# Kernel optimization log

Measured on AMD Instinct MI355X. Metric: run time of the kernel, lower is better.

The kernel has to match this reference:

```python
import jax, jax.numpy as jnp
import numpy as np

N_CODES = 8192
CODE_DIM = 256


def setup_inputs() -> dict:
    key = jax.random.key(0)
    kx, ke = jax.random.split(key)
    x = jax.random.normal(kx, (16, 4096, CODE_DIM), dtype=jnp.float32)
    # nn.Embedding weight initialized uniform(-1/n, 1/n)
    emb = jax.random.uniform(ke, (N_CODES, CODE_DIM), dtype=jnp.float32,
                             minval=-1.0 / N_CODES, maxval=1.0 / N_CODES)
    return {"x": x, "emb": emb}


def reference(x, emb):
    B, T, D = x.shape
    flat = x.reshape(-1, D)                                   # [BT, D]
    # squared euclidean distance: ||f||^2 - 2 f.e^T + ||e||^2  -> [BT, N]
    dist = ((flat * flat).sum(axis=1, keepdims=True)
            - 2.0 * flat @ emb.T
            + (emb * emb).sum(axis=1))
    idx = jnp.argmin(dist, axis=1)                            # [BT] int
    quant = emb[idx].reshape(x.shape)                         # [B, T, D]
    # commitment-style loss: mse(stop_grad(quant), x)
    loss = jnp.mean(jnp.square(jax.lax.stop_gradient(quant) - x))
    # straight-through estimator
    y = x + jax.lax.stop_gradient(quant - x)
    return y, idx.reshape(B, T), loss
```

## Files before the change

kernel.cpp:

```cpp
#include <hip/hip_runtime.h>
#include <stdint.h>


#define NCODES 8192
#define DDIM   256
#define BT     65536

#define TM     128
#define TN     128
#define NSEG   256
#define F4S    17

#define CAPC   48
#define MARGIN 7e-4f
#define TOKPB  128
#define CCODES 64
#define CHUNKS 128
#define KSCALE 1048576.0f
#define KOFF   131072.0f
#define KMARG  737

typedef float  f32x4  __attribute__((ext_vector_type(4)));
typedef __bf16 bf16x8 __attribute__((ext_vector_type(8)));

#define GLDS16(g, l) __builtin_amdgcn_global_load_lds(                         \
    (const __attribute__((address_space(1))) void*)(g),                        \
    (__attribute__((address_space(3))) void*)(l), 16, 0, 0)
#define GLDS4(g, l) __builtin_amdgcn_global_load_lds(                          \
    (const __attribute__((address_space(1))) void*)(g),                        \
    (__attribute__((address_space(3))) void*)(l), 4, 0, 0)

__device__ __forceinline__ unsigned int fenc(float f) {
  unsigned int u = __float_as_uint(f);
  return (u & 0x80000000u) ? ~u : (u | 0x80000000u);
}
__device__ __forceinline__ float fdec(unsigned int u) {
  unsigned int v = (u & 0x80000000u) ? (u ^ 0x80000000u) : ~u;
  return __uint_as_float(v);
}

__device__ __forceinline__ float np_pairwise256_sq(const float4* __restrict__ row) {
#pragma clang fp contract(off)
  float half[2];
  #pragma unroll
  for (int h = 0; h < 2; h++) {
    float r0,r1,r2,r3,r4,r5,r6,r7;
    float4 q0 = row[h*32 + 0];
    float4 q1 = row[h*32 + 1];
    r0 = q0.x*q0.x; r1 = q0.y*q0.y; r2 = q0.z*q0.z; r3 = q0.w*q0.w;
    r4 = q1.x*q1.x; r5 = q1.y*q1.y; r6 = q1.z*q1.z; r7 = q1.w*q1.w;
    #pragma unroll
    for (int g = 1; g < 16; g++) {
      q0 = row[h*32 + g*2];
      q1 = row[h*32 + g*2 + 1];
      r0 += q0.x*q0.x; r1 += q0.y*q0.y; r2 += q0.z*q0.z; r3 += q0.w*q0.w;
      r4 += q1.x*q1.x; r5 += q1.y*q1.y; r6 += q1.z*q1.z; r7 += q1.w*q1.w;
    }
    half[h] = ((r0+r1) + (r2+r3)) + ((r4+r5) + (r6+r7));
  }
  return half[0] + half[1];
}

__device__ __forceinline__ float np_pairwise256_sq_s(const float* __restrict__ row) {
#pragma clang fp contract(off)
  float half[2];
  #pragma unroll
  for (int h = 0; h < 2; h++) {
    const float* p = row + h * 128;
    float r0,r1,r2,r3,r4,r5,r6,r7;
    r0 = p[0]*p[0]; r1 = p[1]*p[1]; r2 = p[2]*p[2]; r3 = p[3]*p[3];
    r4 = p[4]*p[4]; r5 = p[5]*p[5]; r6 = p[6]*p[6]; r7 = p[7]*p[7];
    #pragma unroll
    for (int g = 1; g < 16; g++) {
      const float* q = p + g * 8;
      r0 += q[0]*q[0]; r1 += q[1]*q[1]; r2 += q[2]*q[2]; r3 += q[3]*q[3];
      r4 += q[4]*q[4]; r5 += q[5]*q[5]; r6 += q[6]*q[6]; r7 += q[7]*q[7];
    }
    half[h] = ((r0+r1) + (r2+r3)) + ((r4+r5) + (r6+r7));
  }
  return half[0] + half[1];
}

__device__ __forceinline__ float exact_score(const float* __restrict__ xr,
                                             const float4* __restrict__ er,
                                             float Ar, float Cv) {
#pragma clang fp contract(off)
  float b = 0.0f;
  #pragma unroll 8
  for (int q = 0; q < 64; ++q) {
    float4 ev = er[q];
    b = fmaf(xr[q * 4 + 0], ev.x, b);
    b = fmaf(xr[q * 4 + 1], ev.y, b);
    b = fmaf(xr[q * 4 + 2], ev.z, b);
    b = fmaf(xr[q * 4 + 3], ev.w, b);
  }
  const float t1 = fmaf(-2.0f, b, Ar);
  return t1 + Cv;
}

__device__ __forceinline__ void exact_score2(const float* __restrict__ xr,
                                             const float4* __restrict__ e1,
                                             const float4* __restrict__ e2,
                                             float Ar, float Cv1, float Cv2,
                                             float& s1, float& s2) {
#pragma clang fp contract(off)
  float b1 = 0.0f, b2 = 0.0f;
  #pragma unroll 8
  for (int q = 0; q < 64; ++q) {
    const float4 v1 = e1[q], v2 = e2[q];
    const float x0 = xr[q * 4 + 0], x1 = xr[q * 4 + 1];
    const float x2 = xr[q * 4 + 2], x3 = xr[q * 4 + 3];
    b1 = fmaf(x0, v1.x, b1); b2 = fmaf(x0, v2.x, b2);
    b1 = fmaf(x1, v1.y, b1); b2 = fmaf(x1, v2.y, b2);
    b1 = fmaf(x2, v1.z, b1); b2 = fmaf(x2, v2.z, b2);
    b1 = fmaf(x3, v1.w, b1); b2 = fmaf(x3, v2.w, b2);
  }
  s1 = fmaf(-2.0f, b1, Ar) + Cv1;
  s2 = fmaf(-2.0f, b2, Ar) + Cv2;
}

__global__ void vq_pre_a(const float* __restrict__ x, float* __restrict__ Astage) {
  const int t = blockIdx.x * 256 + threadIdx.x;
  Astage[t] = np_pairwise256_sq((const float4*)(x + (size_t)t * DDIM));
}

__global__ void vq_pre_c(const float* __restrict__ emb, float* __restrict__ Cws) {
  const int c = blockIdx.x * 256 + threadIdx.x;
  Cws[c] = np_pairwise256_sq((const float4*)(emb + (size_t)c * DDIM));
}

__global__ void vq_init(float* __restrict__ oloss) { *oloss = 0.0f; }

__global__ void vq_pre_e(const float* __restrict__ emb, uint4* __restrict__ ebf) {
  const int g   = blockIdx.x * 256 + threadIdx.x;
  const int c   = g >> 5;
  const int blk = g & 31;
  const float4* e4 = (const float4*)(emb + (size_t)c * DDIM);
  float4 f0 = e4[blk*2], f1 = e4[blk*2 + 1];
  union { unsigned short us[8]; uint4 v; } pk;
  pk.us[0] = __builtin_bit_cast(unsigned short, (__bf16)f0.x);
  pk.us[1] = __builtin_bit_cast(unsigned short, (__bf16)f0.y);
  pk.us[2] = __builtin_bit_cast(unsigned short, (__bf16)f0.z);
  pk.us[3] = __builtin_bit_cast(unsigned short, (__bf16)f0.w);
  pk.us[4] = __builtin_bit_cast(unsigned short, (__bf16)f1.x);
  pk.us[5] = __builtin_bit_cast(unsigned short, (__bf16)f1.y);
  pk.us[6] = __builtin_bit_cast(unsigned short, (__bf16)f1.z);
  pk.us[7] = __builtin_bit_cast(unsigned short, (__bf16)f1.w);
  ebf[(size_t)c * 32 + (blk ^ (c & 7))] = pk.v;
}

__device__ __forceinline__ void stage_chunk(const char* __restrict__ ebf,
                                            const float* __restrict__ Cws,
                                            int ch, char* ebuf_dst,
                                            float* cs_dst, int tid) {
  const char* src = ebf + (size_t)ch * 32768 + (size_t)tid * 16;
  char* dst = ebuf_dst + (size_t)tid * 16;
  #pragma unroll
  for (int i = 0; i < 4; ++i) GLDS16(src + i * 8192, dst + i * 8192);
  if (tid < 64)
    GLDS4((const char*)Cws + (size_t)ch * 256 + (size_t)tid * 4,
          (char*)cs_dst + (size_t)tid * 4);
}

__global__ __launch_bounds__(512, 4)
void vq_filter(const float* __restrict__ x, const char* __restrict__ ebf,
               const float* __restrict__ Cws, int* __restrict__ cntG,
               int* __restrict__ candG) {
  __shared__ __align__(16) char ebuf[2][32768];
  __shared__ float Cs[2][64];
  __shared__ unsigned int umin[TOKPB];
  __shared__ int cntL[TOKPB];

  const int tid  = threadIdx.x;
  const int lane = tid & 63;
  const int wid  = tid >> 6;
  const int wm   = wid >> 2;
  const int wn   = wid & 3;
  const int l15  = lane & 15;
  const int lhi  = lane >> 4;
  const int tok0 = blockIdx.x * TOKPB;

  if (tid < TOKPB) { umin[tid] = 0xFFFFFFFFu; cntL[tid] = 0; }

  stage_chunk(ebf, Cws, 0, ebuf[0], Cs[0], tid);

  const float4* x4 = (const float4*)x;
  bf16x8 xb[2][8];
  #pragma unroll
  for (int n = 0; n < 2; ++n) {
    const size_t trow = (size_t)(tok0 + wn * 32 + n * 16 + l15) * 64;
    #pragma unroll
    for (int kk = 0; kk < 8; ++kk) {
      float4 f0 = x4[trow + kk * 8 + lhi * 2];
      float4 f1 = x4[trow + kk * 8 + lhi * 2 + 1];
      bf16x8 v;
      v[0] = (__bf16)f0.x; v[1] = (__bf16)f0.y; v[2] = (__bf16)f0.z; v[3] = (__bf16)f0.w;
      v[4] = (__bf16)f1.x; v[5] = (__bf16)f1.y; v[6] = (__bf16)f1.z; v[7] = (__bf16)f1.w;
      xb[n][kk] = v;
    }
  }
  __syncthreads();

  const f32x4 zf = {0.f, 0.f, 0.f, 0.f};
  float rmin[2] = {1e30f, 1e30f};

  for (int c = 0; c < CHUNKS; ++c) {
    stage_chunk(ebf, Cws, (c + 1) & (CHUNKS - 1), ebuf[(c + 1) & 1],
                Cs[(c + 1) & 1], tid);

    const char* ecur = ebuf[c & 1];
    f32x4 acc[2][2];
    #pragma unroll
    for (int kk = 0; kk < 8; ++kk) {
      bf16x8 a[2];
      #pragma unroll
      for (int m = 0; m < 2; ++m) {
        const int row = wm * 32 + m * 16 + l15;
        const int blk = (kk * 4 + lhi) ^ (row & 7);
        a[m] = *(const bf16x8*)(ecur + row * 512 + blk * 16);
      }
      #pragma unroll
      for (int m = 0; m < 2; ++m)
        #pragma unroll
        for (int n = 0; n < 2; ++n)
          acc[m][n] = __builtin_amdgcn_mfma_f32_16x16x32_bf16(
              a[m], xb[n][kk], (kk == 0) ? zf : acc[m][n], 0, 0, 0);
    }

    const float* Csc = Cs[c & 1];
    float cvals[2][4];
    #pragma unroll
    for (int m = 0; m < 2; ++m)
      #pragma unroll
      for (int r = 0; r < 4; ++r)
        cvals[m][r] = Csc[wm * 32 + m * 16 + lhi * 4 + r];

    #pragma unroll
    for (int n = 0; n < 2; ++n) {
      const int t = wn * 32 + n * 16 + l15;
      float s[8];
      float mn = 1e30f;
      #pragma unroll
      for (int m = 0; m < 2; ++m)
        #pragma unroll
        for (int r = 0; r < 4; ++r) {
          const float v = fmaf(-2.0f, acc[m][n][r], cvals[m][r]);
          s[m * 4 + r] = v;
          mn = fminf(mn, v);
        }
      mn = fminf(mn, __shfl_xor(mn, 16));
      mn = fminf(mn, __shfl_xor(mn, 32));
      if (mn < rmin[n]) {
        rmin[n] = mn;
        if (lhi == 0) atomicMin(&umin[t], fenc(mn));
      }
      const float thr = fminf(rmin[n], fdec(umin[t])) + MARGIN;
      #pragma unroll
      for (int m = 0; m < 2; ++m)
        #pragma unroll
        for (int r = 0; r < 4; ++r) {
          if (s[m * 4 + r] <= thr) {
            const int code = c * CCODES + wm * 32 + m * 16 + lhi * 4 + r;
            int key = (int)fmaf(s[m * 4 + r], KSCALE, KOFF);
            key = min(max(key, 0), 262143);
            const int pos = atomicAdd(&cntL[t], 1);
            if (pos < CAPC)
              candG[(size_t)(tok0 + t) * CAPC + pos] = (key << 13) | code;
          }
        }
    }

    __syncthreads();
  }

  if (tid < TOKPB) cntG[tok0 + tid] = cntL[tid];
}

__global__ __launch_bounds__(256, 2)
void vq_rescore(const float* __restrict__ x, const float* __restrict__ emb,
                const float* __restrict__ Cws, const int* __restrict__ cntG,
                const int* __restrict__ candG, float* __restrict__ y,
                float* __restrict__ oidx, float* __restrict__ oloss) {
  __shared__ float xs[64 * 257];
  __shared__ float As[64];
  __shared__ int   idx_sh[64];
  __shared__ float red[4];
  __shared__ float rbv[256];
  __shared__ int   rbi[256];
  __shared__ int   ovf_list[64];
  __shared__ int   n_ovf;

  const int tid  = threadIdx.x;
  const int tok0 = blockIdx.x * 64;
  const float4* x4g = (const float4*)x;
  const float4* e4g = (const float4*)emb;

  if (tid == 0) n_ovf = 0;
  #pragma unroll
  for (int i = 0; i < 16; ++i) {
    const int g = tid + 256 * i, row = g >> 6, c4 = g & 63;
    float4 v = x4g[(size_t)(tok0 + row) * 64 + c4];
    float* p = &xs[row * 257 + c4 * 4];
    p[0] = v.x; p[1] = v.y; p[2] = v.z; p[3] = v.w;
  }
  __syncthreads();
  if (tid < 64) As[tid] = np_pairwise256_sq_s(&xs[tid * 257]);
  __syncthreads();

  const int t  = tid >> 2;
  const int j0 = tid & 3;
  const int gt = tok0 + t;
  const int cnt = cntG[gt];
  const float* xr = &xs[t * 257];
  const float  Ar = As[t];

  if (cnt <= CAPC) {
    int pmin = 0x7FFFFFFF;
    for (int j = j0; j < cnt; j += 4) pmin = min(pmin, candG[(size_t)gt * CAPC + j]);
    pmin = min(pmin, __shfl_xor(pmin, 1));
    pmin = min(pmin, __shfl_xor(pmin, 2));
    const int thrk = (pmin >> 13) + KMARG;
    float best = 1e30f; int bid = 0x7FFFFFFF;
    for (int j = j0; j < cnt; j += 4) {
      const int e = candG[(size_t)gt * CAPC + j];
      if ((e >> 13) <= thrk) {
        const int c = e & 8191;
        const float s = exact_score(xr, e4g + (size_t)c * 64, Ar, Cws[c]);
        if (s < best || (s == best && c < bid)) { best = s; bid = c; }
      }
    }
    #pragma unroll
    for (int off = 1; off <= 2; off <<= 1) {
      const float ob = __shfl_xor(best, off);
      const int   oi = __shfl_xor(bid, off);
      if (ob < best || (ob == best && oi < bid)) { best = ob; bid = oi; }
    }
    if (j0 == 0) { idx_sh[t] = bid; oidx[gt] = (float)(bid + 1); }
  } else if (j0 == 0) {
    const int p = atomicAdd(&n_ovf, 1);
    ovf_list[p] = t;
  }
  __syncthreads();

  for (int o = 0; o < n_ovf; ++o) {
    const int tt  = ovf_list[o];
    const float* xrr = &xs[tt * 257];
    const float  At  = As[tt];
    float bv = 1e30f; int bi2 = 0x7FFFFFFF;
    for (int c0 = tid; c0 < NCODES; c0 += 512) {
      const int c1 = c0 + 256;
      float s1, s2;
      exact_score2(xrr, e4g + (size_t)c0 * 64, e4g + (size_t)c1 * 64,
                   At, Cws[c0], Cws[c1], s1, s2);
      if (s1 < bv || (s1 == bv && c0 < bi2)) { bv = s1; bi2 = c0; }
      if (s2 < bv || (s2 == bv && c1 < bi2)) { bv = s2; bi2 = c1; }
    }
    rbv[tid] = bv; rbi[tid] = bi2;
    __syncthreads();
    #pragma unroll
    for (int sft = 128; sft; sft >>= 1) {
      if (tid < sft) {
        const float v2 = rbv[tid + sft]; const int i2 = rbi[tid + sft];
        if (v2 < rbv[tid] || (v2 == rbv[tid] && i2 < rbi[tid])) {
          rbv[tid] = v2; rbi[tid] = i2;
        }
      }
      __syncthreads();
    }
    if (tid == 0) { idx_sh[tt] = rbi[0]; oidx[tok0 + tt] = (float)(rbi[0] + 1); }
    __syncthreads();
  }
  __syncthreads();

  float lsum = 0.0f;
  float4* y4 = (float4*)y;
  #pragma unroll
  for (int r = 0; r < 16; ++r) {
    const int g = tid + 256 * r, row = g >> 6, c4 = g & 63;
    const float4 ev = e4g[(size_t)idx_sh[row] * 64 + c4];
    const float4 xv = x4g[(size_t)(tok0 + row) * 64 + c4];
    y4[(size_t)(tok0 + row) * 64 + c4] = ev;
    const float dx = ev.x - xv.x, dy = ev.y - xv.y, dz = ev.z - xv.z, dw = ev.w - xv.w;
    lsum += dx * dx + dy * dy + dz * dz + dw * dw;
  }
  #pragma unroll
  for (int off = 32; off; off >>= 1) lsum += __shfl_down(lsum, off);
  if ((tid & 63) == 0) red[tid >> 6] = lsum;
  __syncthreads();
  if (tid == 0) atomicAdd(oloss, red[0] + red[1] + red[2] + red[3]);
}

__global__ void vq_fin(float* __restrict__ oloss) {
  *oloss = *oloss * (1.0f / 16777216.0f);
}

__global__ __launch_bounds__(256, 2)
void vq_main(const float* __restrict__ x, const float* __restrict__ emb,
             const float* __restrict__ Cws, float* __restrict__ y,
             float* __restrict__ oidx, float* __restrict__ oloss) {
  __shared__ float4 xs4[TM * F4S];
  __shared__ float4 es4[TN * F4S];
  __shared__ float  Cs[TN];
  __shared__ int    idx_sh[TM];
  __shared__ float  red[4];

  const int tid = threadIdx.x;
  const int ry = tid >> 4;
  const int rx = tid & 15;
  const int tok0 = blockIdx.x * TM;

  const float4* x4g = (const float4*)x;
  const float4* e4g = (const float4*)emb;

  float A_reg[8];
  #pragma unroll
  for (int m = 0; m < 8; m++) A_reg[m] = oidx[tok0 + ry + 16 * m];

  float best[8];
  int   i1[8];
  #pragma unroll
  for (int m = 0; m < 8; m++) { best[m] = 1e30f; i1[m] = 0; }

  float acc[8][8];

  for (int seg = 0; seg < NSEG; ++seg) {
    const int chunk = seg >> 2;
    const int kq = seg & 3;
    __syncthreads();
    #pragma unroll
    for (int h = 0; h < 2; h++) {
      float4 t[4];
      #pragma unroll
      for (int q = 0; q < 4; q++) {
        const int r = h * 4 + q;
        t[q] = x4g[(size_t)(tok0 + ry + 16 * r) * 64 + kq * 16 + rx];
      }
      #pragma unroll
      for (int q = 0; q < 4; q++) {
        const int r = h * 4 + q;
        xs4[(ry + 16 * r) * F4S + rx] = t[q];
      }
    }
    #pragma unroll
    for (int h = 0; h < 2; h++) {
      float4 t[4];
      #pragma unroll
      for (int q = 0; q < 4; q++) {
        const int r = h * 4 + q;
        t[q] = e4g[(size_t)(chunk * TN + ry + 16 * r) * 64 + kq * 16 + rx];
      }
      #pragma unroll
      for (int q = 0; q < 4; q++) {
        const int r = h * 4 + q;
        es4[(ry + 16 * r) * F4S + rx] = t[q];
      }
    }
    if (kq == 0 && tid < TN) Cs[tid] = Cws[chunk * TN + tid];
    __syncthreads();

    if (kq == 0) {
      #pragma unroll
      for (int m = 0; m < 8; m++)
        #pragma unroll
        for (int n = 0; n < 8; n++) acc[m][n] = 0.0f;
    }

    #pragma unroll
    for (int k4 = 0; k4 < 16; k4++) {
      float4 a[8], b[8];
      #pragma unroll
      for (int m = 0; m < 8; m++) a[m] = xs4[(ry + 16 * m) * F4S + k4];
      #pragma unroll
      for (int n = 0; n < 8; n++) b[n] = es4[(rx + 16 * n) * F4S + k4];
      #pragma unroll
      for (int m = 0; m < 8; m++)
        #pragma unroll
        for (int n = 0; n < 8; n++) {
          acc[m][n] = fmaf(a[m].x, b[n].x, acc[m][n]);
          acc[m][n] = fmaf(a[m].y, b[n].y, acc[m][n]);
          acc[m][n] = fmaf(a[m].z, b[n].z, acc[m][n]);
          acc[m][n] = fmaf(a[m].w, b[n].w, acc[m][n]);
        }
    }

    if (kq == 3) {
      const int c0 = chunk * TN;
      #pragma unroll
      for (int n = 0; n < 8; n++) {
        const float Cv = Cs[rx + 16 * n];
        const int c = c0 + rx + 16 * n;
        #pragma unroll
        for (int m = 0; m < 8; m++) {
          const float t1 = fmaf(-2.0f, acc[m][n], A_reg[m]);
          const float t2 = t1 + Cv;
          if (t2 < best[m]) { best[m] = t2; i1[m] = c; }
        }
      }
    }
  }

  __syncthreads();
  float* bv1 = (float*)xs4;
  int*   bi  = (int*)es4;
  #pragma unroll
  for (int m = 0; m < 8; m++) {
    bv1[(ry + 16 * m) * 16 + rx] = best[m];
    bi [(ry + 16 * m) * 16 + rx] = i1[m];
  }
  __syncthreads();
  if (tid < TM) {
    float v = bv1[tid * 16];
    int   id = bi[tid * 16];
    for (int t = 1; t < 16; t++) {
      const float vv = bv1[tid * 16 + t];
      const int   ii = bi [tid * 16 + t];
      if (vv < v || (vv == v && ii < id)) { v = vv; id = ii; }
    }
    idx_sh[tid] = id;
    oidx[tok0 + tid] = (float)(id + 1);
  }
  __syncthreads();

  float lsum = 0.0f;
  float4* y4 = (float4*)y;
  #pragma unroll
  for (int r = 0; r < 32; r++) {
    const int g = tid + 256 * r, row = g >> 6, c4 = g & 63;
    const float4 ev = e4g[(size_t)idx_sh[row] * 64 + c4];
    const float4 xv = x4g[(size_t)(tok0 + row) * 64 + c4];
    y4[(size_t)(tok0 + row) * 64 + c4] = ev;
    const float dx = ev.x - xv.x, dy = ev.y - xv.y, dz = ev.z - xv.z, dw = ev.w - xv.w;
    lsum += dx * dx + dy * dy + dz * dz + dw * dw;
  }
  #pragma unroll
  for (int off = 32; off; off >>= 1) lsum += __shfl_down(lsum, off);
  if ((tid & 63) == 0) red[tid >> 6] = lsum;
  __syncthreads();
  if (tid == 0) atomicAdd(oloss, red[0] + red[1] + red[2] + red[3]);
}

extern "C" void kernel_launch(void* const* d_in, const int* in_sizes, int n_in,
                              void* d_out, int out_size, void* d_ws, size_t ws_size,
                              hipStream_t stream) {
  const float* x   = (const float*)d_in[0];
  const float* emb = (const float*)d_in[1];

  float* y     = (float*)d_out;
  float* oidx  = y + (size_t)BT * DDIM;
  float* oloss = oidx + BT;

  char*  wsB   = (char*)d_ws;
  float* Cws   = (float*)wsB;
  int*   cntG  = (int*)(wsB + 32768);
  char*  ebf   = wsB + 32768 + 262144;
  int*   candG = (int*)(wsB + 294912 + 4194304);
  const size_t NEED = 294912 + 4194304 + (size_t)BT * CAPC * 4;

  vq_init <<<1, 1,           0, stream>>>(oloss);
  vq_pre_c<<<NCODES/256,256, 0, stream>>>(emb, Cws);

  if (ws_size >= NEED) {
    vq_pre_e  <<<1024, 256, 0, stream>>>(emb, (uint4*)ebf);
    vq_filter <<<BT/TOKPB, 512, 0, stream>>>(x, ebf, Cws, cntG, candG);
    vq_rescore<<<1024, 256, 0, stream>>>(x, emb, Cws, cntG, candG, y, oidx, oloss);
  } else {
    vq_pre_a<<<BT / 256, 256, 0, stream>>>(x, oidx);
    vq_main <<<BT / TM, 256,  0, stream>>>(x, emb, Cws, y, oidx, oloss);
  }
  vq_fin  <<<1, 1,           0, stream>>>(oloss);
}
```

Baseline: 769.6 us.

## Fuse rescore stage into filter kernel using rotated LDS x tile

Merges the separate rescore kernel into the tail of the bf16 MFMA filter kernel. Candidate counts stay in shared memory instead of a global array, and the x rows are staged into the now-free codebook LDS buffer with a rotated layout that avoids bank conflicts. The change drops one kernel launch and the global round trip of the per-token counts. It also removes the useless prefetch on the last iteration. In exchange, the rescore phase now runs at the filter kernel's 512-thread occupancy and processes two 64-token halves serially per block, with a rotated indexing scheme that adds address arithmetic.

```diff
diff --git a/kernel.cpp b/kernel.cpp
--- a/kernel.cpp
+++ b/kernel.cpp
@@ -61,59 +61,65 @@
   return half[0] + half[1];
 }
 
-__device__ __forceinline__ float np_pairwise256_sq_s(const float* __restrict__ row) {
+__device__ __forceinline__ const float4* rot_blk(const char* base, int t, int q) {
+  return (const float4*)(base + (size_t)t * 1024 + (size_t)(((q - t) & 63) << 4));
+}
+
+__device__ __forceinline__ float np_pairwise256_rot(const char* xb, int t) {
 #pragma clang fp contract(off)
   float half[2];
   #pragma unroll
   for (int h = 0; h < 2; h++) {
-    const float* p = row + h * 128;
     float r0,r1,r2,r3,r4,r5,r6,r7;
-    r0 = p[0]*p[0]; r1 = p[1]*p[1]; r2 = p[2]*p[2]; r3 = p[3]*p[3];
-    r4 = p[4]*p[4]; r5 = p[5]*p[5]; r6 = p[6]*p[6]; r7 = p[7]*p[7];
+    float4 q0 = *rot_blk(xb, t, h*32 + 0);
+    float4 q1 = *rot_blk(xb, t, h*32 + 1);
+    r0 = q0.x*q0.x; r1 = q0.y*q0.y; r2 = q0.z*q0.z; r3 = q0.w*q0.w;
+    r4 = q1.x*q1.x; r5 = q1.y*q1.y; r6 = q1.z*q1.z; r7 = q1.w*q1.w;
     #pragma unroll
     for (int g = 1; g < 16; g++) {
-      const float* q = p + g * 8;
-      r0 += q[0]*q[0]; r1 += q[1]*q[1]; r2 += q[2]*q[2]; r3 += q[3]*q[3];
-      r4 += q[4]*q[4]; r5 += q[5]*q[5]; r6 += q[6]*q[6]; r7 += q[7]*q[7];
+      q0 = *rot_blk(xb, t, h*32 + g*2);
+      q1 = *rot_blk(xb, t, h*32 + g*2 + 1);
+      r0 += q0.x*q0.x; r1 += q0.y*q0.y; r2 += q0.z*q0.z; r3 += q0.w*q0.w;
+      r4 += q1.x*q1.x; r5 += q1.y*q1.y; r6 += q1.z*q1.z; r7 += q1.w*q1.w;
     }
     half[h] = ((r0+r1) + (r2+r3)) + ((r4+r5) + (r6+r7));
   }
   return half[0] + half[1];
 }
 
-__device__ __forceinline__ float exact_score(const float* __restrict__ xr,
-                                             const float4* __restrict__ er,
-                                             float Ar, float Cv) {
+__device__ __forceinline__ float exact_score_rot(const char* xb, int t,
+                                                 const float4* __restrict__ er,
+                                                 float Ar, float Cv) {
 #pragma clang fp contract(off)
   float b = 0.0f;
   #pragma unroll 8
   for (int q = 0; q < 64; ++q) {
-    float4 ev = er[q];
-    b = fmaf(xr[q * 4 + 0], ev.x, b);
-    b = fmaf(xr[q * 4 + 1], ev.y, b);
-    b = fmaf(xr[q * 4 + 2], ev.z, b);
-    b = fmaf(xr[q * 4 + 3], ev.w, b);
+    const float4 xv = *rot_blk(xb, t, q);
+    const float4 ev = er[q];
+    b = fmaf(xv.x, ev.x, b);
+    b = fmaf(xv.y, ev.y, b);
+    b = fmaf(xv.z, ev.z, b);
+    b = fmaf(xv.w, ev.w, b);
   }
   const float t1 = fmaf(-2.0f, b, Ar);
   return t1 + Cv;
 }
 
-__device__ __forceinline__ void exact_score2(const float* __restrict__ xr,
-                                             const float4* __restrict__ e1,
-                                             const float4* __restrict__ e2,
-                                             float Ar, float Cv1, float Cv2,
-                                             float& s1, float& s2) {
+__device__ __forceinline__ void exact_score2_rot(const char* xb, int t,
+                                                 const float4* __restrict__ e1,
+                                                 const float4* __restrict__ e2,
+                                                 float Ar, float Cv1, float Cv2,
+                                                 float& s1, float& s2) {
 #pragma clang fp contract(off)
   float b1 = 0.0f, b2 = 0.0f;
   #pragma unroll 8
   for (int q = 0; q < 64; ++q) {
+    const float4 xv = *rot_blk(xb, t, q);
     const float4 v1 = e1[q], v2 = e2[q];
-    const float x0 = xr[q * 4 + 0], x1 = xr[q * 4 + 1];
-    const float x2 = xr[q * 4 + 2], x3 = xr[q * 4 + 3];
-    b1 = fmaf(x0, v1.x, b1); b2 = fmaf(x0, v2.x, b2);
-    b1 = fmaf(x1, v1.y, b1); b2 = fmaf(x1, v2.y, b2);
-    b1 = fmaf(x2, v1.z, b1); b2 = fmaf(x2, v2.z, b2);
-    b1 = fmaf(x3, v1.w, b1); b2 = fmaf(x3, v2.w, b2);
+    b1 = fmaf(xv.x, v1.x, b1); b2 = fmaf(xv.x, v2.x, b2);
+    b1 = fmaf(xv.y, v1.y, b1); b2 = fmaf(xv.y, v2.y, b2);
+    b1 = fmaf(xv.z, v1.z, b1); b2 = fmaf(xv.z, v2.z, b2);
+    b1 = fmaf(xv.w, v1.w, b1); b2 = fmaf(xv.w, v2.w, b2);
   }
   s1 = fmaf(-2.0f, b1, Ar) + Cv1;
   s2 = fmaf(-2.0f, b2, Ar) + Cv2;
@@ -163,13 +169,21 @@
 }
 
 __global__ __launch_bounds__(512, 4)
-void vq_filter(const float* __restrict__ x, const char* __restrict__ ebf,
-               const float* __restrict__ Cws, int* __restrict__ cntG,
-               int* __restrict__ candG) {
+void vq_filter(const float* __restrict__ x, const float* __restrict__ emb,
+               const char* __restrict__ ebf, const float* __restrict__ Cws,
+               int* __restrict__ candG, float* __restrict__ y,
+               float* __restrict__ oidx, float* __restrict__ oloss) {
   __shared__ __align__(16) char ebuf[2][32768];
   __shared__ float Cs[2][64];
   __shared__ unsigned int umin[TOKPB];
   __shared__ int cntL[TOKPB];
+  __shared__ float As_sh[64];
+  __shared__ int   idx_sh[64];
+  __shared__ int   ovf_list[64];
+  __shared__ int   n_ovf;
+  __shared__ float wbv[8];
+  __shared__ int   wbi[8];
+  __shared__ float red[8];
 
   const int tid  = threadIdx.x;
   const int lane = tid & 63;
@@ -205,8 +219,8 @@
   float rmin[2] = {1e30f, 1e30f};
 
   for (int c = 0; c < CHUNKS; ++c) {
-    stage_chunk(ebf, Cws, (c + 1) & (CHUNKS - 1), ebuf[(c + 1) & 1],
-                Cs[(c + 1) & 1], tid);
+    if (c + 1 < CHUNKS)
+      stage_chunk(ebf, Cws, c + 1, ebuf[(c + 1) & 1], Cs[(c + 1) & 1], tid);
 
     const char* ecur = ebuf[c & 1];
     f32x4 acc[2][2];
@@ -273,121 +287,123 @@
     __syncthreads();
   }
 
-  if (tid < TOKPB) cntG[tok0 + tid] = cntL[tid];
-}
-
-__global__ __launch_bounds__(256, 2)
-void vq_rescore(const float* __restrict__ x, const float* __restrict__ emb,
-                const float* __restrict__ Cws, const int* __restrict__ cntG,
-                const int* __restrict__ candG, float* __restrict__ y,
-                float* __restrict__ oidx, float* __restrict__ oloss) {
-  __shared__ float xs[64 * 257];
-  __shared__ float As[64];
-  __shared__ int   idx_sh[64];
-  __shared__ float red[4];
-  __shared__ float rbv[256];
-  __shared__ int   rbi[256];
-  __shared__ int   ovf_list[64];
-  __shared__ int   n_ovf;
-
-  const int tid  = threadIdx.x;
-  const int tok0 = blockIdx.x * 64;
-  const float4* x4g = (const float4*)x;
   const float4* e4g = (const float4*)emb;
-
-  if (tid == 0) n_ovf = 0;
-  #pragma unroll
-  for (int i = 0; i < 16; ++i) {
-    const int g = tid + 256 * i, row = g >> 6, c4 = g & 63;
-    float4 v = x4g[(size_t)(tok0 + row) * 64 + c4];
-    float* p = &xs[row * 257 + c4 * 4];
-    p[0] = v.x; p[1] = v.y; p[2] = v.z; p[3] = v.w;
-  }
+  const char* xls = (const char*)ebuf;
+  float lsum = 0.0f;
+
+  for (int h = 0; h < 2; ++h) {
+    __syncthreads();
+    if (tid == 0) n_ovf = 0;
+    {
+      const int tbase = tok0 + h * 64;
+      #pragma unroll
+      for (int i = 0; i < 8; ++i) {
+        const int u = tid + 512 * i;
+        const int t = u >> 6, s = u & 63, q = (s + t) & 63;
+        GLDS16(x + (size_t)(tbase + t) * 256 + q * 4,
+               (char*)ebuf + (size_t)u * 16);
+      }
+    }
+    __syncthreads();
+    if (tid < 64) As_sh[tid] = np_pairwise256_rot(xls, tid);
+    __syncthreads();
+
+    const int t  = tid >> 3;
+    const int j0 = tid & 7;
+    const int gt = tok0 + h * 64 + t;
+    const int cnt = cntL[h * 64 + t];
+    const float Ar = As_sh[t];
+
+    if (cnt <= CAPC) {
+      int pmin = 0x7FFFFFFF;
+      for (int j = j0; j < cnt; j += 8)
+        pmin = min(pmin, candG[(size_t)gt * CAPC + j]);
+      pmin = min(pmin, __shfl_xor(pmin, 1));
+      pmin = min(pmin, __shfl_xor(pmin, 2));
+      pmin = min(pmin, __shfl_xor(pmin, 4));
+      const int thrk = (pmin >> 13) + KMARG;
+      float best = 1e30f; int bid = 0x7FFFFFFF;
+      for (int j = j0; j < cnt; j += 8) {
+        const int e = candG[(size_t)gt * CAPC + j];
+        if ((e >> 13) <= thrk) {
+          const int c = e & 8191;
+          const float s = exact_score_rot(xls, t, e4g + (size_t)c * 64,
+                                          Ar, Cws[c]);
+          if (s < best || (s == best && c < bid)) { best = s; bid = c; }
+        }
+      }
+      #pragma unroll
+      for (int off = 1; off <= 4; off <<= 1) {
+        const float ob = __shfl_xor(best, off);
+        const int   oi = __shfl_xor(bid, off);
+        if (ob < best || (ob == best && oi < bid)) { best = ob; bid = oi; }
+      }
+      if (j0 == 0) { idx_sh[t] = bid; oidx[gt] = (float)(bid + 1); }
+    } else if (j0 == 0) {
+      ovf_list[atomicAdd(&n_ovf, 1)] = t;
+    }
+    __syncthreads();
+
+    for (int o = 0; o < n_ovf; ++o) {
+      const int tt = ovf_list[o];
+      const float At = As_sh[tt];
+      float bv = 1e30f; int bi2 = 0x7FFFFFFF;
+      for (int c0 = tid; c0 < NCODES; c0 += 1024) {
+        const int c1 = c0 + 512;
+        float s1, s2;
+        exact_score2_rot(xls, tt, e4g + (size_t)c0 * 64, e4g + (size_t)c1 * 64,
+                         At, Cws[c0], Cws[c1], s1, s2);
+        if (s1 < bv || (s1 == bv && c0 < bi2)) { bv = s1; bi2 = c0; }
+        if (s2 < bv || (s2 == bv && c1 < bi2)) { bv = s2; bi2 = c1; }
+      }
+      #pragma unroll
+      for (int off = 1; off <= 32; off <<= 1) {
+        const float ob = __shfl_xor(bv, off);
+        const int   oi = __shfl_xor(bi2, off);
+        if (ob < bv || (ob == bv && oi < bi2)) { bv = ob; bi2 = oi; }
+      }
+      if (lane == 0) { wbv[wid] = bv; wbi[wid] = bi2; }
+      __syncthreads();
+      if (tid == 0) {
+        float fb = wbv[0]; int fi = wbi[0];
+        #pragma unroll
+        for (int w = 1; w < 8; ++w)
+          if (wbv[w] < fb || (wbv[w] == fb && wbi[w] < fi)) {
+            fb = wbv[w]; fi = wbi[w];
+          }
+        idx_sh[tt] = fi;
+        oidx[tok0 + h * 64 + tt] = (float)(fi + 1);
+      }
+      __syncthreads();
+    }
+
+    {
+      float4* y4 = (float4*)y;
+      const int tbase = tok0 + h * 64;
+      #pragma unroll
+      for (int i = 0; i < 8; ++i) {
+        const int u = tid + 512 * i;
+        const int row = u >> 6, pos = u & 63;
+        const float4 ev = e4g[(size_t)idx_sh[row] * 64 + pos];
+        const float4 xv = *rot_blk(xls, row, pos);
+        y4[(size_t)(tbase + row) * 64 + pos] = ev;
+        const float dx = ev.x - xv.x, dy = ev.y - xv.y,
+                    dz = ev.z - xv.z, dw = ev.w - xv.w;
+        lsum += dx * dx + dy * dy + dz * dz + dw * dw;
+      }
+    }
+  }
+
+  #pragma unroll
+  for (int off = 32; off; off >>= 1) lsum += __shfl_down(lsum, off);
+  if (lane == 0) red[wid] = lsum;
   __syncthreads();
-  if (tid < 64) As[tid] = np_pairwise256_sq_s(&xs[tid * 257]);
-  __syncthreads();
-
-  const int t  = tid >> 2;
-  const int j0 = tid & 3;
-  const int gt = tok0 + t;
-  const int cnt = cntG[gt];
-  const float* xr = &xs[t * 257];
-  const float  Ar = As[t];
-
-  if (cnt <= CAPC) {
-    int pmin = 0x7FFFFFFF;
-    for (int j = j0; j < cnt; j += 4) pmin = min(pmin, candG[(size_t)gt * CAPC + j]);
-    pmin = min(pmin, __shfl_xor(pmin, 1));
-    pmin = min(pmin, __shfl_xor(pmin, 2));
-    const int thrk = (pmin >> 13) + KMARG;
-    float best = 1e30f; int bid = 0x7FFFFFFF;
-    for (int j = j0; j < cnt; j += 4) {
-      const int e = candG[(size_t)gt * CAPC + j];
-      if ((e >> 13) <= thrk) {
-        const int c = e & 8191;
-        const float s = exact_score(xr, e4g + (size_t)c * 64, Ar, Cws[c]);
-        if (s < best || (s == best && c < bid)) { best = s; bid = c; }
-      }
-    }
-    #pragma unroll
-    for (int off = 1; off <= 2; off <<= 1) {
-      const float ob = __shfl_xor(best, off);
-      const int   oi = __shfl_xor(bid, off);
-      if (ob < best || (ob == best && oi < bid)) { best = ob; bid = oi; }
-    }
-    if (j0 == 0) { idx_sh[t] = bid; oidx[gt] = (float)(bid + 1); }
-  } else if (j0 == 0) {
-    const int p = atomicAdd(&n_ovf, 1);
-    ovf_list[p] = t;
-  }
-  __syncthreads();
-
-  for (int o = 0; o < n_ovf; ++o) {
-    const int tt  = ovf_list[o];
-    const float* xrr = &xs[tt * 257];
-    const float  At  = As[tt];
-    float bv = 1e30f; int bi2 = 0x7FFFFFFF;
-    for (int c0 = tid; c0 < NCODES; c0 += 512) {
-      const int c1 = c0 + 256;
-      float s1, s2;
-      exact_score2(xrr, e4g + (size_t)c0 * 64, e4g + (size_t)c1 * 64,
-                   At, Cws[c0], Cws[c1], s1, s2);
-      if (s1 < bv || (s1 == bv && c0 < bi2)) { bv = s1; bi2 = c0; }
-      if (s2 < bv || (s2 == bv && c1 < bi2)) { bv = s2; bi2 = c1; }
-    }
-    rbv[tid] = bv; rbi[tid] = bi2;
-    __syncthreads();
-    #pragma unroll
-    for (int sft = 128; sft; sft >>= 1) {
-      if (tid < sft) {
-        const float v2 = rbv[tid + sft]; const int i2 = rbi[tid + sft];
-        if (v2 < rbv[tid] || (v2 == rbv[tid] && i2 < rbi[tid])) {
-          rbv[tid] = v2; rbi[tid] = i2;
-        }
-      }
-      __syncthreads();
-    }
-    if (tid == 0) { idx_sh[tt] = rbi[0]; oidx[tok0 + tt] = (float)(rbi[0] + 1); }
-    __syncthreads();
-  }
-  __syncthreads();
-
-  float lsum = 0.0f;
-  float4* y4 = (float4*)y;
-  #pragma unroll
-  for (int r = 0; r < 16; ++r) {
-    const int g = tid + 256 * r, row = g >> 6, c4 = g & 63;
-    const float4 ev = e4g[(size_t)idx_sh[row] * 64 + c4];
-    const float4 xv = x4g[(size_t)(tok0 + row) * 64 + c4];
-    y4[(size_t)(tok0 + row) * 64 + c4] = ev;
-    const float dx = ev.x - xv.x, dy = ev.y - xv.y, dz = ev.z - xv.z, dw = ev.w - xv.w;
-    lsum += dx * dx + dy * dy + dz * dz + dw * dw;
-  }
-  #pragma unroll
-  for (int off = 32; off; off >>= 1) lsum += __shfl_down(lsum, off);
-  if ((tid & 63) == 0) red[tid >> 6] = lsum;
-  __syncthreads();
-  if (tid == 0) atomicAdd(oloss, red[0] + red[1] + red[2] + red[3]);
+  if (tid == 0) {
+    float s = 0.0f;
+    #pragma unroll
+    for (int w = 0; w < 8; ++w) s += red[w];
+    atomicAdd(oloss, s);
+  }
 }
 
 __global__ void vq_fin(float* __restrict__ oloss) {
@@ -551,7 +567,6 @@
 
   char*  wsB   = (char*)d_ws;
   float* Cws   = (float*)wsB;
-  int*   cntG  = (int*)(wsB + 32768);
   char*  ebf   = wsB + 32768 + 262144;
   int*   candG = (int*)(wsB + 294912 + 4194304);
   const size_t NEED = 294912 + 4194304 + (size_t)BT * CAPC * 4;
@@ -560,9 +575,9 @@
   vq_pre_c<<<NCODES/256,256, 0, stream>>>(emb, Cws);
 
   if (ws_size >= NEED) {
-    vq_pre_e  <<<1024, 256, 0, stream>>>(emb, (uint4*)ebf);
-    vq_filter <<<BT/TOKPB, 512, 0, stream>>>(x, ebf, Cws, cntG, candG);
-    vq_rescore<<<1024, 256, 0, stream>>>(x, emb, Cws, cntG, candG, y, oidx, oloss);
+    vq_pre_e <<<1024, 256, 0, stream>>>(emb, (uint4*)ebf);
+    vq_filter<<<BT/TOKPB, 512, 0, stream>>>(x, emb, ebf, Cws, candG,
+                                            y, oidx, oloss);
   } else {
     vq_pre_a<<<BT / 256, 256, 0, stream>>>(x, oidx);
     vq_main <<<BT / TM, 256,  0, stream>>>(x, emb, Cws, y, oidx, oloss);
```

After: 842.8 us. 9.5% more time.

## Skip exact rescoring for single-candidate tokens and drop shared x staging

Applied to the files above, without the earlier changes.

The rescoring kernel no longer stages each 64-token tile of x into a 64 KB shared buffer and no longer precomputes row norms up front. It first counts the candidates within the key margin, and when only one survives it writes that code directly without any exact dot products. Otherwise it computes the row norm lazily and scores candidates by reading x straight from global memory. The smaller shared footprint allows raising the launch bound to 4 blocks per SM. The cost is that each of the 4 lanes per token rereads x from global or L2 instead of from LDS.

```diff
diff --git a/kernel.cpp b/kernel.cpp
--- a/kernel.cpp
+++ b/kernel.cpp
@@ -61,59 +61,39 @@
   return half[0] + half[1];
 }
 
-__device__ __forceinline__ float np_pairwise256_sq_s(const float* __restrict__ row) {
-#pragma clang fp contract(off)
-  float half[2];
-  #pragma unroll
-  for (int h = 0; h < 2; h++) {
-    const float* p = row + h * 128;
-    float r0,r1,r2,r3,r4,r5,r6,r7;
-    r0 = p[0]*p[0]; r1 = p[1]*p[1]; r2 = p[2]*p[2]; r3 = p[3]*p[3];
-    r4 = p[4]*p[4]; r5 = p[5]*p[5]; r6 = p[6]*p[6]; r7 = p[7]*p[7];
-    #pragma unroll
-    for (int g = 1; g < 16; g++) {
-      const float* q = p + g * 8;
-      r0 += q[0]*q[0]; r1 += q[1]*q[1]; r2 += q[2]*q[2]; r3 += q[3]*q[3];
-      r4 += q[4]*q[4]; r5 += q[5]*q[5]; r6 += q[6]*q[6]; r7 += q[7]*q[7];
-    }
-    half[h] = ((r0+r1) + (r2+r3)) + ((r4+r5) + (r6+r7));
-  }
-  return half[0] + half[1];
-}
-
-__device__ __forceinline__ float exact_score(const float* __restrict__ xr,
-                                             const float4* __restrict__ er,
-                                             float Ar, float Cv) {
+__device__ __forceinline__ float exact_score_g(const float4* __restrict__ xr,
+                                               const float4* __restrict__ er,
+                                               float Ar, float Cv) {
 #pragma clang fp contract(off)
   float b = 0.0f;
   #pragma unroll 8
   for (int q = 0; q < 64; ++q) {
-    float4 ev = er[q];
-    b = fmaf(xr[q * 4 + 0], ev.x, b);
-    b = fmaf(xr[q * 4 + 1], ev.y, b);
-    b = fmaf(xr[q * 4 + 2], ev.z, b);
-    b = fmaf(xr[q * 4 + 3], ev.w, b);
+    const float4 xv = xr[q];
+    const float4 ev = er[q];
+    b = fmaf(xv.x, ev.x, b);
+    b = fmaf(xv.y, ev.y, b);
+    b = fmaf(xv.z, ev.z, b);
+    b = fmaf(xv.w, ev.w, b);
   }
   const float t1 = fmaf(-2.0f, b, Ar);
   return t1 + Cv;
 }
 
-__device__ __forceinline__ void exact_score2(const float* __restrict__ xr,
-                                             const float4* __restrict__ e1,
-                                             const float4* __restrict__ e2,
-                                             float Ar, float Cv1, float Cv2,
-                                             float& s1, float& s2) {
+__device__ __forceinline__ void exact_score2_g(const float4* __restrict__ xr,
+                                               const float4* __restrict__ e1,
+                                               const float4* __restrict__ e2,
+                                               float Ar, float Cv1, float Cv2,
+                                               float& s1, float& s2) {
 #pragma clang fp contract(off)
   float b1 = 0.0f, b2 = 0.0f;
   #pragma unroll 8
   for (int q = 0; q < 64; ++q) {
+    const float4 xv = xr[q];
     const float4 v1 = e1[q], v2 = e2[q];
-    const float x0 = xr[q * 4 + 0], x1 = xr[q * 4 + 1];
-    const float x2 = xr[q * 4 + 2], x3 = xr[q * 4 + 3];
-    b1 = fmaf(x0, v1.x, b1); b2 = fmaf(x0, v2.x, b2);
-    b1 = fmaf(x1, v1.y, b1); b2 = fmaf(x1, v2.y, b2);
-    b1 = fmaf(x2, v1.z, b1); b2 = fmaf(x2, v2.z, b2);
-    b1 = fmaf(x3, v1.w, b1); b2 = fmaf(x3, v2.w, b2);
+    b1 = fmaf(xv.x, v1.x, b1); b2 = fmaf(xv.x, v2.x, b2);
+    b1 = fmaf(xv.y, v1.y, b1); b2 = fmaf(xv.y, v2.y, b2);
+    b1 = fmaf(xv.z, v1.z, b1); b2 = fmaf(xv.z, v2.z, b2);
+    b1 = fmaf(xv.w, v1.w, b1); b2 = fmaf(xv.w, v2.w, b2);
   }
   s1 = fmaf(-2.0f, b1, Ar) + Cv1;
   s2 = fmaf(-2.0f, b2, Ar) + Cv2;
@@ -276,19 +256,17 @@
   if (tid < TOKPB) cntG[tok0 + tid] = cntL[tid];
 }
 
-__global__ __launch_bounds__(256, 2)
-void vq_rescore(const float* __restrict__ x, const float* __restrict__ emb,
-                const float* __restrict__ Cws, const int* __restrict__ cntG,
-                const int* __restrict__ candG, float* __restrict__ y,
-                float* __restrict__ oidx, float* __restrict__ oloss) {
-  __shared__ float xs[64 * 257];
-  __shared__ float As[64];
+__global__ __launch_bounds__(256, 4)
+void vq_finalize(const float* __restrict__ x, const float* __restrict__ emb,
+                 const float* __restrict__ Cws, const int* __restrict__ cntG,
+                 const int* __restrict__ candG, float* __restrict__ y,
+                 float* __restrict__ oidx, float* __restrict__ oloss) {
   __shared__ int   idx_sh[64];
-  __shared__ float red[4];
+  __shared__ int   ovf_list[64];
+  __shared__ int   n_ovf;
   __shared__ float rbv[256];
   __shared__ int   rbi[256];
-  __shared__ int   ovf_list[64];
-  __shared__ int   n_ovf;
+  __shared__ float red[4];
 
   const int tid  = threadIdx.x;
   const int tok0 = blockIdx.x * 64;
@@ -296,62 +274,68 @@
   const float4* e4g = (const float4*)emb;
 
   if (tid == 0) n_ovf = 0;
-  #pragma unroll
-  for (int i = 0; i < 16; ++i) {
-    const int g = tid + 256 * i, row = g >> 6, c4 = g & 63;
-    float4 v = x4g[(size_t)(tok0 + row) * 64 + c4];
-    float* p = &xs[row * 257 + c4 * 4];
-    p[0] = v.x; p[1] = v.y; p[2] = v.z; p[3] = v.w;
-  }
-  __syncthreads();
-  if (tid < 64) As[tid] = np_pairwise256_sq_s(&xs[tid * 257]);
   __syncthreads();
 
   const int t  = tid >> 2;
   const int j0 = tid & 3;
   const int gt = tok0 + t;
   const int cnt = cntG[gt];
-  const float* xr = &xs[t * 257];
-  const float  Ar = As[t];
+  const float4* xr = x4g + (size_t)gt * 64;
 
   if (cnt <= CAPC) {
     int pmin = 0x7FFFFFFF;
-    for (int j = j0; j < cnt; j += 4) pmin = min(pmin, candG[(size_t)gt * CAPC + j]);
+    for (int j = j0; j < cnt; j += 4)
+      pmin = min(pmin, candG[(size_t)gt * CAPC + j]);
     pmin = min(pmin, __shfl_xor(pmin, 1));
     pmin = min(pmin, __shfl_xor(pmin, 2));
     const int thrk = (pmin >> 13) + KMARG;
-    float best = 1e30f; int bid = 0x7FFFFFFF;
+    int nsv = 0, smin = 0x7FFFFFFF;
     for (int j = j0; j < cnt; j += 4) {
       const int e = candG[(size_t)gt * CAPC + j];
-      if ((e >> 13) <= thrk) {
-        const int c = e & 8191;
-        const float s = exact_score(xr, e4g + (size_t)c * 64, Ar, Cws[c]);
-        if (s < best || (s == best && c < bid)) { best = s; bid = c; }
-      }
-    }
-    #pragma unroll
-    for (int off = 1; off <= 2; off <<= 1) {
-      const float ob = __shfl_xor(best, off);
-      const int   oi = __shfl_xor(bid, off);
-      if (ob < best || (ob == best && oi < bid)) { best = ob; bid = oi; }
-    }
-    if (j0 == 0) { idx_sh[t] = bid; oidx[gt] = (float)(bid + 1); }
+      if ((e >> 13) <= thrk) { nsv++; smin = min(smin, e); }
+    }
+    nsv += __shfl_xor(nsv, 1);
+    nsv += __shfl_xor(nsv, 2);
+    smin = min(smin, __shfl_xor(smin, 1));
+    smin = min(smin, __shfl_xor(smin, 2));
+
+    if (nsv == 1) {
+      if (j0 == 0) { idx_sh[t] = smin & 8191; oidx[gt] = (float)((smin & 8191) + 1); }
+    } else {
+      float best = 1e30f; int bid = 0x7FFFFFFF;
+      float Ar = 0.0f; bool haveA = false;
+      for (int j = j0; j < cnt; j += 4) {
+        const int e = candG[(size_t)gt * CAPC + j];
+        if ((e >> 13) <= thrk) {
+          if (!haveA) { Ar = np_pairwise256_sq(xr); haveA = true; }
+          const int c = e & 8191;
+          const float s = exact_score_g(xr, e4g + (size_t)c * 64, Ar, Cws[c]);
+          if (s < best || (s == best && c < bid)) { best = s; bid = c; }
+        }
+      }
+      #pragma unroll
+      for (int off = 1; off <= 2; off <<= 1) {
+        const float ob = __shfl_xor(best, off);
+        const int   oi = __shfl_xor(bid, off);
+        if (ob < best || (ob == best && oi < bid)) { best = ob; bid = oi; }
+      }
+      if (j0 == 0) { idx_sh[t] = bid; oidx[gt] = (float)(bid + 1); }
+    }
   } else if (j0 == 0) {
-    const int p = atomicAdd(&n_ovf, 1);
-    ovf_list[p] = t;
+    ovf_list[atomicAdd(&n_ovf, 1)] = t;
   }
   __syncthreads();
 
   for (int o = 0; o < n_ovf; ++o) {
-    const int tt  = ovf_list[o];
-    const float* xrr = &xs[tt * 257];
-    const float  At  = As[tt];
+    const int tt = ovf_list[o];
+    const float4* xrr = x4g + (size_t)(tok0 + tt) * 64;
+    const float At = np_pairwise256_sq(xrr);
     float bv = 1e30f; int bi2 = 0x7FFFFFFF;
     for (int c0 = tid; c0 < NCODES; c0 += 512) {
       const int c1 = c0 + 256;
       float s1, s2;
-      exact_score2(xrr, e4g + (size_t)c0 * 64, e4g + (size_t)c1 * 64,
-                   At, Cws[c0], Cws[c1], s1, s2);
+      exact_score2_g(xrr, e4g + (size_t)c0 * 64, e4g + (size_t)c1 * 64,
+                     At, Cws[c0], Cws[c1], s1, s2);
       if (s1 < bv || (s1 == bv && c0 < bi2)) { bv = s1; bi2 = c0; }
       if (s2 < bv || (s2 == bv && c1 < bi2)) { bv = s2; bi2 = c1; }
     }
@@ -560,9 +544,10 @@
   vq_pre_c<<<NCODES/256,256, 0, stream>>>(emb, Cws);
 
   if (ws_size >= NEED) {
-    vq_pre_e  <<<1024, 256, 0, stream>>>(emb, (uint4*)ebf);
-    vq_filter <<<BT/TOKPB, 512, 0, stream>>>(x, ebf, Cws, cntG, candG);
-    vq_rescore<<<1024, 256, 0, stream>>>(x, emb, Cws, cntG, candG, y, oidx, oloss);
+    vq_pre_e   <<<1024, 256, 0, stream>>>(emb, (uint4*)ebf);
+    vq_filter  <<<BT/TOKPB, 512, 0, stream>>>(x, ebf, Cws, cntG, candG);
+    vq_finalize<<<BT/64, 256, 0, stream>>>(x, emb, Cws, cntG, candG,
+                                           y, oidx, oloss);
   } else {
     vq_pre_a<<<BT / 256, 256, 0, stream>>>(x, oidx);
     vq_main <<<BT / TM, 256,  0, stream>>>(x, emb, Cws, y, oidx, oloss);
```

New measurement: 866.0 us. +12.5%, slower.
